# Kernel tuning notes

Measured on AMD Instinct MI355X. Metric: run time of the kernel, lower is better.

## Reference

```python
import jax, jax.numpy as jnp
import numpy as np

K_LAYERS = 10
ALPHA = 0.1
N_NODES = 100_000
N_EDGES = 1_600_000
D_FEAT = 64


def setup_inputs() -> dict:
    key = jax.random.key(0)
    k1, k2, k3 = jax.random.split(key, 3)
    features = jax.random.normal(k1, (N_NODES, D_FEAT), dtype=jnp.float32)
    src = jax.random.randint(k2, (N_EDGES,), 0, N_NODES, dtype=jnp.int64)
    dst = jax.random.randint(k3, (N_EDGES,), 0, N_NODES, dtype=jnp.int64)
    return {"features": features, "src": src, "dst": dst}


def reference(features, src, dst):
    # APPNP forward (eval mode: feature dropout and edge_drop are identity).
    n = features.shape[0]
    ones = jnp.ones((src.shape[0],), dtype=features.dtype)
    deg_out = jax.ops.segment_sum(ones, src, num_segments=n)
    deg_in = jax.ops.segment_sum(ones, dst, num_segments=n)
    norm_src = jnp.clip(deg_out, 1.0) ** -0.5  # [N]
    norm_dst = jnp.clip(deg_in, 1.0) ** -0.5   # [N]

    h0 = features
    h = features
    for _ in range(K_LAYERS):
        # D_out^{-1/2} scaling, gather to edges, scatter-sum to dst, D_in^{-1/2}
        msg = (h * norm_src[:, None])[src]               # [E, d]
        agg = jax.ops.segment_sum(msg, dst, num_segments=n)  # [N, d]
        h = (1.0 - ALPHA) * (agg * norm_dst[:, None]) + ALPHA * h0
    return h
```

## Files before the change

kernel.cpp:

```cpp
#include <hip/hip_runtime.h>
#include <hip/hip_fp16.h>
#include <stdint.h>

#define D_FEAT 64
#define K_LAYERS 10
#define SCAN_CHUNK 2048

__global__ void deg_kernel(const int* __restrict__ src, const int* __restrict__ dst,
                           int* deg_out, int* deg_in, int* __restrict__ rank, int E) {
    int i = blockIdx.x * blockDim.x + threadIdx.x;
    int base = i * 4;
    if (base + 3 < E) {
        int4 s4 = *(const int4*)(src + base);
        int4 d4 = *(const int4*)(dst + base);
        atomicAdd(&deg_out[s4.x], 1);
        atomicAdd(&deg_out[s4.y], 1);
        atomicAdd(&deg_out[s4.z], 1);
        atomicAdd(&deg_out[s4.w], 1);
        int4 r;
        r.x = atomicAdd(&deg_in[d4.x], 1);
        r.y = atomicAdd(&deg_in[d4.y], 1);
        r.z = atomicAdd(&deg_in[d4.z], 1);
        r.w = atomicAdd(&deg_in[d4.w], 1);
        *(int4*)(rank + base) = r;
    } else {
        for (int j = base; j < E; ++j) {
            atomicAdd(&deg_out[src[j]], 1);
            rank[j] = atomicAdd(&deg_in[dst[j]], 1);
        }
    }
}

__global__ void norm_kernel(const int* __restrict__ deg_out, const int* __restrict__ deg_in,
                            float* __restrict__ ns, float* __restrict__ nd,
                            float* __restrict__ cvec, int N) {
    int i = blockIdx.x * blockDim.x + threadIdx.x;
    if (i < N) {
        float a = rsqrtf(fmaxf((float)deg_out[i], 1.0f));
        float b = rsqrtf(fmaxf((float)deg_in[i], 1.0f));
        ns[i] = a;
        nd[i] = b;
        cvec[i] = 0.9f * a * b;
    }
}

__global__ void chunk_sum_kernel(const int* __restrict__ deg, int N, int* __restrict__ partials) {
    __shared__ int sdata[256];
    constexpr int PT = SCAN_CHUNK / 256;
    int base = blockIdx.x * SCAN_CHUNK;
    int t = threadIdx.x;
    int s = 0;
#pragma unroll
    for (int j = 0; j < PT; ++j) {
        int idx = base + t * PT + j;
        if (idx < N) s += deg[idx];
    }
    sdata[t] = s;
    __syncthreads();
    for (int off = 128; off > 0; off >>= 1) {
        if (t < off) sdata[t] += sdata[t + off];
        __syncthreads();
    }
    if (t == 0) partials[blockIdx.x] = sdata[0];
}

__global__ void scan_partials_kernel(int* partials, int nchunks, int* row_ptr, int N, int E) {
    if (threadIdx.x == 0 && blockIdx.x == 0) {
        int s = 0;
        for (int i = 0; i < nchunks; ++i) { int v = partials[i]; partials[i] = s; s += v; }
        row_ptr[N] = E;
    }
}

__global__ void chunk_scan_kernel(const int* __restrict__ deg, int N,
                                  const int* __restrict__ partials, int* __restrict__ row_ptr) {
    __shared__ int sdata[256];
    constexpr int PT = SCAN_CHUNK / 256;
    int base = blockIdx.x * SCAN_CHUNK;
    int t = threadIdx.x;
    int vals[PT];
    int s = 0;
#pragma unroll
    for (int j = 0; j < PT; ++j) {
        int idx = base + t * PT + j;
        int v = (idx < N) ? deg[idx] : 0;
        vals[j] = s;
        s += v;
    }
    sdata[t] = s;
    __syncthreads();
    for (int off = 1; off < 256; off <<= 1) {
        int v = (t >= off) ? sdata[t - off] : 0;
        __syncthreads();
        sdata[t] += v;
        __syncthreads();
    }
    int texcl = (t > 0) ? sdata[t - 1] : 0;
    int off0 = partials[blockIdx.x];
#pragma unroll
    for (int j = 0; j < PT; ++j) {
        int idx = base + t * PT + j;
        if (idx < N) row_ptr[idx] = off0 + texcl + vals[j];
    }
}

__global__ void fill_cvt_kernel(const int* __restrict__ src, const int* __restrict__ dst,
                                const int* __restrict__ rank, const int* __restrict__ row_ptr,
                                unsigned* __restrict__ edge_src, int E, int fillBlocks,
                                const float* __restrict__ features, const float* __restrict__ ns,
                                __half* __restrict__ g0, __half* __restrict__ f0g, int N) {
    int b = blockIdx.x;
    if (b < fillBlocks) {
        int i = b * blockDim.x + threadIdx.x;
        int base = i * 4;
        if (base + 3 < E) {
            int4 s4 = *(const int4*)(src + base);
            int4 d4 = *(const int4*)(dst + base);
            int4 r4 = *(const int4*)(rank + base);
            edge_src[row_ptr[d4.x] + r4.x] = (unsigned)s4.x;
            edge_src[row_ptr[d4.y] + r4.y] = (unsigned)s4.y;
            edge_src[row_ptr[d4.z] + r4.z] = (unsigned)s4.z;
            edge_src[row_ptr[d4.w] + r4.w] = (unsigned)s4.w;
        } else {
            for (int j = base; j < E; ++j)
                edge_src[row_ptr[dst[j]] + rank[j]] = (unsigned)src[j];
        }
    } else {
        int t = (b - fillBlocks) * blockDim.x + threadIdx.x;
        if (t < N * (D_FEAT / 8)) {
            int node = t >> 3;
            float s = ns[node];
            float4 a = *((const float4*)features + 2 * t);
            float4 c = *((const float4*)features + 2 * t + 1);
            __half2 og[4], of[4];
        og[0] = __float22half2_rn(make_float2(s * a.x, s * a.y));
        og[1] = __float22half2_rn(make_float2(s * a.z, s * a.w));
        og[2] = __float22half2_rn(make_float2(s * c.x, s * c.y));
        og[3] = __float22half2_rn(make_float2(s * c.z, s * c.w));
        float sf = 0.1f * s;
        of[0] = __float22half2_rn(make_float2(sf * a.x, sf * a.y));
        of[1] = __float22half2_rn(make_float2(sf * a.z, sf * a.w));
        of[2] = __float22half2_rn(make_float2(sf * c.x, sf * c.y));
        of[3] = __float22half2_rn(make_float2(sf * c.z, sf * c.w));
            *((float4*)g0 + t)  = *(const float4*)og;
            *((float4*)f0g + t) = *(const float4*)of;
        }
    }
}

template <bool LAST>
__global__ __launch_bounds__(256) void prop_kernel(
    const __half* __restrict__ g, const __half* __restrict__ f0g,
    const float* __restrict__ features,
    const unsigned* __restrict__ edge_src, const int* __restrict__ row_ptr,
    const float* __restrict__ cvec, const float* __restrict__ nd,
    void* __restrict__ out, int N)
{
    int gid  = blockIdx.x * blockDim.x + threadIdx.x;
    int node = gid >> 6;
    if (node >= N) return;
    int lane = threadIdx.x & 63;
    int grp  = lane >> 3;
    int fl   = lane & 7;

    int start = row_ptr[node];
    int end   = row_ptr[node + 1];

    float acc[8];
#pragma unroll
    for (int j = 0; j < 8; ++j) acc[j] = 0.f;

    int e = start + grp;
    for (; e + 8 < end; e += 16) {
        unsigned s0 = edge_src[e];
        unsigned s1 = edge_src[e + 8];
        float4 v0 = *((const float4*)(g + ((size_t)s0 << 6)) + fl);
        float4 v1 = *((const float4*)(g + ((size_t)s1 << 6)) + fl);
        const __half2* p0 = (const __half2*)&v0;
        const __half2* p1 = (const __half2*)&v1;
#pragma unroll
        for (int k = 0; k < 4; ++k) {
            float2 f0 = __half22float2(p0[k]);
            float2 f1 = __half22float2(p1[k]);
            acc[2 * k]     += f0.x + f1.x;
            acc[2 * k + 1] += f0.y + f1.y;
        }
    }
    if (e < end) {
        unsigned s0 = edge_src[e];
        float4 v0 = *((const float4*)(g + ((size_t)s0 << 6)) + fl);
        const __half2* p0 = (const __half2*)&v0;
#pragma unroll
        for (int k = 0; k < 4; ++k) {
            float2 f0 = __half22float2(p0[k]);
            acc[2 * k]     += f0.x;
            acc[2 * k + 1] += f0.y;
        }
    }

#pragma unroll
    for (int j = 0; j < 8; ++j) acc[j] += __shfl_xor(acc[j], 8, 64);
#pragma unroll
    for (int j = 0; j < 8; ++j) acc[j] += __shfl_xor(acc[j], 16, 64);
#pragma unroll
    for (int j = 0; j < 8; ++j) acc[j] += __shfl_xor(acc[j], 32, 64);

    if (grp == 0) {
        if (!LAST) {
            float cm = cvec[node];
            float4 braw = *((const float4*)(f0g + ((size_t)node << 6)) + fl);
            const __half2* bp = (const __half2*)&braw;
            __half2 o[4];
#pragma unroll
            for (int k = 0; k < 4; ++k) {
                float2 f = __half22float2(bp[k]);
                o[k] = __float22half2_rn(make_float2(fmaf(cm, acc[2 * k], f.x),
                                                     fmaf(cm, acc[2 * k + 1], f.y)));
            }
            *((float4*)((__half*)out + ((size_t)node << 6)) + fl) = *(const float4*)o;
        } else {
            float w = 0.9f * nd[node];
            const float4* fp = (const float4*)(features + ((size_t)node << 6));
            float4 b0 = fp[2 * fl];
            float4 b1 = fp[2 * fl + 1];
            float4 o0, o1;
            o0.x = fmaf(w, acc[0], 0.1f * b0.x);
            o0.y = fmaf(w, acc[1], 0.1f * b0.y);
            o0.z = fmaf(w, acc[2], 0.1f * b0.z);
            o0.w = fmaf(w, acc[3], 0.1f * b0.w);
            o1.x = fmaf(w, acc[4], 0.1f * b1.x);
            o1.y = fmaf(w, acc[5], 0.1f * b1.y);
            o1.z = fmaf(w, acc[6], 0.1f * b1.z);
            o1.w = fmaf(w, acc[7], 0.1f * b1.w);
            float4* op = (float4*)((float*)out + ((size_t)node << 6));
            op[2 * fl]     = o0;
            op[2 * fl + 1] = o1;
        }
    }
}

extern "C" void kernel_launch(void* const* d_in, const int* in_sizes, int n_in,
                              void* d_out, int out_size, void* d_ws, size_t ws_size,
                              hipStream_t stream) {
    const float* features = (const float*)d_in[0];
    const int*   src      = (const int*)d_in[1];
    const int*   dst      = (const int*)d_in[2];
    const int E = in_sizes[1];
    const int N = in_sizes[0] / D_FEAT;

    char* ws = (char*)d_ws;
    size_t off = 0;
    auto alloc = [&](size_t bytes, size_t align) -> char* {
        off = (off + align - 1) & ~(align - 1);
        char* p = ws + off;
        off += bytes;
        return p;
    };
    int*      deg_out  = (int*)alloc(4 * (size_t)N, 4);
    int*      deg_in   = (int*)alloc(4 * (size_t)N, 4);
    int*      row_ptr  = (int*)alloc(4 * ((size_t)N + 1), 4);
    float*    ns       = (float*)alloc(4 * (size_t)N, 4);
    float*    nd       = (float*)alloc(4 * (size_t)N, 4);
    float*    cvec     = (float*)alloc(4 * (size_t)N, 4);
    int nchunks = (N + SCAN_CHUNK - 1) / SCAN_CHUNK;
    int*      partials = (int*)alloc(4 * (size_t)nchunks, 4);
    int*      rank     = (int*)alloc(4 * (size_t)E, 16);
    unsigned* edge_src = (unsigned*)alloc(4 * (size_t)E, 16);
    __half*   f0g      = (__half*)alloc(2 * (size_t)N * D_FEAT, 16);
    __half*   gA       = (__half*)alloc(2 * (size_t)N * D_FEAT, 16);
    __half*   gB       = (__half*)alloc(2 * (size_t)N * D_FEAT, 16);

    hipMemsetAsync(deg_out, 0, 4 * (size_t)N * 2, stream);

    int ethreads4 = (E + 3) / 4;
    int eblocks = (ethreads4 + 255) / 256;
    deg_kernel<<<eblocks, 256, 0, stream>>>(src, dst, deg_out, deg_in, rank, E);
    norm_kernel<<<(N + 255) / 256, 256, 0, stream>>>(deg_out, deg_in, ns, nd, cvec, N);
    chunk_sum_kernel<<<nchunks, 256, 0, stream>>>(deg_in, N, partials);
    scan_partials_kernel<<<1, 64, 0, stream>>>(partials, nchunks, row_ptr, N, E);
    chunk_scan_kernel<<<nchunks, 256, 0, stream>>>(deg_in, N, partials, row_ptr);

    int cvtThreads = N * (D_FEAT / 8);
    int cvtBlocks = (cvtThreads + 255) / 256;
    fill_cvt_kernel<<<eblocks + cvtBlocks, 256, 0, stream>>>(
        src, dst, rank, row_ptr, edge_src, E, eblocks, features, ns, gA, f0g, N);

    int prop_blocks = (int)(((size_t)N * 64 + 255) / 256);
    const __half* h_in = gA;
    for (int k = 0; k < K_LAYERS - 1; ++k) {
        __half* h_out = (k & 1) ? gA : gB;
        prop_kernel<false><<<prop_blocks, 256, 0, stream>>>(
            h_in, f0g, features, edge_src, row_ptr, cvec, nd, h_out, N);
        h_in = h_out;
    }
    prop_kernel<true><<<prop_blocks, 256, 0, stream>>>(
        h_in, f0g, features, edge_src, row_ptr, cvec, nd, d_out, N);
}
```

Measured before the change: 728.8 us.

## Use LDS histogram for out-degree and map one node per 8-lane group

Out-degree counting moves from global atomics to 32 dedicated blocks that build per-block LDS histograms over node ranges, writing partial counts that norm_kernel sums. The in-degree and rank atomics run in other blocks of the same launch. The propagation kernel now gives each 8-lane group its own node instead of a whole 64-lane wave per node, which removes the cross-group shuffle reduction and the idle lanes on nodes with few edges. In exchange, it adds a 32×N partials buffer, repeated passes over the src stripes, and more load imbalance within a wave.

```diff
diff --git a/kernel.cpp b/kernel.cpp
--- a/kernel.cpp
+++ b/kernel.cpp
@@ -5,42 +5,76 @@
 #define D_FEAT 64
 #define K_LAYERS 10
 #define SCAN_CHUNK 2048
-
-__global__ void deg_kernel(const int* __restrict__ src, const int* __restrict__ dst,
-                           int* deg_out, int* deg_in, int* __restrict__ rank, int E) {
-    int i = blockIdx.x * blockDim.x + threadIdx.x;
-    int base = i * 4;
-    if (base + 3 < E) {
-        int4 s4 = *(const int4*)(src + base);
-        int4 d4 = *(const int4*)(dst + base);
-        atomicAdd(&deg_out[s4.x], 1);
-        atomicAdd(&deg_out[s4.y], 1);
-        atomicAdd(&deg_out[s4.z], 1);
-        atomicAdd(&deg_out[s4.w], 1);
-        int4 r;
-        r.x = atomicAdd(&deg_in[d4.x], 1);
-        r.y = atomicAdd(&deg_in[d4.y], 1);
-        r.z = atomicAdd(&deg_in[d4.z], 1);
-        r.w = atomicAdd(&deg_in[d4.w], 1);
-        *(int4*)(rank + base) = r;
+#define HIST_BLOCKS 32
+#define HIST_RANGE 16384
+
+__global__ void deg_hist_kernel(const int* __restrict__ src, const int* __restrict__ dst,
+                                int* deg_in, int* __restrict__ rank,
+                                unsigned* __restrict__ partials, int E, int histBlocks, int N) {
+    __shared__ unsigned lds[HIST_RANGE];
+    int b = blockIdx.x;
+    if (b >= histBlocks) {
+        int i = (b - histBlocks) * blockDim.x + threadIdx.x;
+        int base = i * 4;
+        if (base + 3 < E) {
+            int4 d4 = *(const int4*)(dst + base);
+            int4 r;
+            r.x = atomicAdd(&deg_in[d4.x], 1);
+            r.y = atomicAdd(&deg_in[d4.y], 1);
+            r.z = atomicAdd(&deg_in[d4.z], 1);
+            r.w = atomicAdd(&deg_in[d4.w], 1);
+            *(int4*)(rank + base) = r;
+        } else {
+            for (int j = base; j < E; ++j)
+                rank[j] = atomicAdd(&deg_in[dst[j]], 1);
+        }
     } else {
-        for (int j = base; j < E; ++j) {
-            atomicAdd(&deg_out[src[j]], 1);
-            rank[j] = atomicAdd(&deg_in[dst[j]], 1);
-        }
-    }
-}
-
-__global__ void norm_kernel(const int* __restrict__ deg_out, const int* __restrict__ deg_in,
+        int stripe = ((E + histBlocks - 1) / histBlocks + 3) & ~3;
+        int begin = b * stripe;
+        int endb  = min(E, begin + stripe);
+        int nr = (N + HIST_RANGE - 1) / HIST_RANGE;
+        for (int r = 0; r < nr; ++r) {
+            for (int j = threadIdx.x; j < HIST_RANGE; j += blockDim.x) lds[j] = 0;
+            __syncthreads();
+            unsigned lo = (unsigned)(r * HIST_RANGE);
+            for (int p = begin + (int)threadIdx.x * 4; p < endb; p += blockDim.x * 4) {
+                if (p + 3 < endb) {
+                    int4 s4 = *(const int4*)(src + p);
+                    unsigned k;
+                    k = (unsigned)s4.x - lo; if (k < HIST_RANGE) atomicAdd(&lds[k], 1u);
+                    k = (unsigned)s4.y - lo; if (k < HIST_RANGE) atomicAdd(&lds[k], 1u);
+                    k = (unsigned)s4.z - lo; if (k < HIST_RANGE) atomicAdd(&lds[k], 1u);
+                    k = (unsigned)s4.w - lo; if (k < HIST_RANGE) atomicAdd(&lds[k], 1u);
+                } else {
+                    for (int q = p; q < endb; ++q) {
+                        unsigned k = (unsigned)src[q] - lo;
+                        if (k < HIST_RANGE) atomicAdd(&lds[k], 1u);
+                    }
+                }
+            }
+            __syncthreads();
+            for (int j = threadIdx.x; j < HIST_RANGE; j += blockDim.x) {
+                int gi = r * HIST_RANGE + j;
+                if (gi < N) partials[(size_t)b * N + gi] = lds[j];
+            }
+            __syncthreads();
+        }
+    }
+}
+
+__global__ void norm_kernel(const unsigned* __restrict__ partials, const int* __restrict__ deg_in,
                             float* __restrict__ ns, float* __restrict__ nd,
                             float* __restrict__ cvec, int N) {
     int i = blockIdx.x * blockDim.x + threadIdx.x;
     if (i < N) {
-        float a = rsqrtf(fmaxf((float)deg_out[i], 1.0f));
-        float b = rsqrtf(fmaxf((float)deg_in[i], 1.0f));
+        unsigned s = 0;
+#pragma unroll 8
+        for (int b = 0; b < HIST_BLOCKS; ++b) s += partials[(size_t)b * N + i];
+        float a = rsqrtf(fmaxf((float)s, 1.0f));
+        float bb = rsqrtf(fmaxf((float)deg_in[i], 1.0f));
         ns[i] = a;
-        nd[i] = b;
-        cvec[i] = 0.9f * a * b;
+        nd[i] = bb;
+        cvec[i] = 0.9f * a * bb;
     }
 }
 
@@ -133,15 +167,15 @@
             float4 a = *((const float4*)features + 2 * t);
             float4 c = *((const float4*)features + 2 * t + 1);
             __half2 og[4], of[4];
-        og[0] = __float22half2_rn(make_float2(s * a.x, s * a.y));
-        og[1] = __float22half2_rn(make_float2(s * a.z, s * a.w));
-        og[2] = __float22half2_rn(make_float2(s * c.x, s * c.y));
-        og[3] = __float22half2_rn(make_float2(s * c.z, s * c.w));
-        float sf = 0.1f * s;
-        of[0] = __float22half2_rn(make_float2(sf * a.x, sf * a.y));
-        of[1] = __float22half2_rn(make_float2(sf * a.z, sf * a.w));
-        of[2] = __float22half2_rn(make_float2(sf * c.x, sf * c.y));
-        of[3] = __float22half2_rn(make_float2(sf * c.z, sf * c.w));
+            og[0] = __float22half2_rn(make_float2(s * a.x, s * a.y));
+            og[1] = __float22half2_rn(make_float2(s * a.z, s * a.w));
+            og[2] = __float22half2_rn(make_float2(s * c.x, s * c.y));
+            og[3] = __float22half2_rn(make_float2(s * c.z, s * c.w));
+            float sf = 0.1f * s;
+            of[0] = __float22half2_rn(make_float2(sf * a.x, sf * a.y));
+            of[1] = __float22half2_rn(make_float2(sf * a.z, sf * a.w));
+            of[2] = __float22half2_rn(make_float2(sf * c.x, sf * c.y));
+            of[3] = __float22half2_rn(make_float2(sf * c.z, sf * c.w));
             *((float4*)g0 + t)  = *(const float4*)og;
             *((float4*)f0g + t) = *(const float4*)of;
         }
@@ -156,24 +190,24 @@
     const float* __restrict__ cvec, const float* __restrict__ nd,
     void* __restrict__ out, int N)
 {
-    int gid  = blockIdx.x * blockDim.x + threadIdx.x;
-    int node = gid >> 6;
-    if (node >= N) return;
+    int tid  = blockIdx.x * blockDim.x + threadIdx.x;
+    int wave = tid >> 6;
     int lane = threadIdx.x & 63;
     int grp  = lane >> 3;
     int fl   = lane & 7;
-
-    int start = row_ptr[node];
-    int end   = row_ptr[node + 1];
+    int node = wave * 8 + grp;
+    if (node >= N) return;
+
+    int e   = row_ptr[node];
+    int end = row_ptr[node + 1];
 
     float acc[8];
 #pragma unroll
     for (int j = 0; j < 8; ++j) acc[j] = 0.f;
 
-    int e = start + grp;
-    for (; e + 8 < end; e += 16) {
+    for (; e + 2 <= end; e += 2) {
         unsigned s0 = edge_src[e];
-        unsigned s1 = edge_src[e + 8];
+        unsigned s1 = edge_src[e + 1];
         float4 v0 = *((const float4*)(g + ((size_t)s0 << 6)) + fl);
         float4 v1 = *((const float4*)(g + ((size_t)s1 << 6)) + fl);
         const __half2* p0 = (const __half2*)&v0;
@@ -198,44 +232,35 @@
         }
     }
 
-#pragma unroll
-    for (int j = 0; j < 8; ++j) acc[j] += __shfl_xor(acc[j], 8, 64);
-#pragma unroll
-    for (int j = 0; j < 8; ++j) acc[j] += __shfl_xor(acc[j], 16, 64);
-#pragma unroll
-    for (int j = 0; j < 8; ++j) acc[j] += __shfl_xor(acc[j], 32, 64);
-
-    if (grp == 0) {
-        if (!LAST) {
-            float cm = cvec[node];
-            float4 braw = *((const float4*)(f0g + ((size_t)node << 6)) + fl);
-            const __half2* bp = (const __half2*)&braw;
-            __half2 o[4];
-#pragma unroll
-            for (int k = 0; k < 4; ++k) {
-                float2 f = __half22float2(bp[k]);
-                o[k] = __float22half2_rn(make_float2(fmaf(cm, acc[2 * k], f.x),
-                                                     fmaf(cm, acc[2 * k + 1], f.y)));
-            }
-            *((float4*)((__half*)out + ((size_t)node << 6)) + fl) = *(const float4*)o;
-        } else {
-            float w = 0.9f * nd[node];
-            const float4* fp = (const float4*)(features + ((size_t)node << 6));
-            float4 b0 = fp[2 * fl];
-            float4 b1 = fp[2 * fl + 1];
-            float4 o0, o1;
-            o0.x = fmaf(w, acc[0], 0.1f * b0.x);
-            o0.y = fmaf(w, acc[1], 0.1f * b0.y);
-            o0.z = fmaf(w, acc[2], 0.1f * b0.z);
-            o0.w = fmaf(w, acc[3], 0.1f * b0.w);
-            o1.x = fmaf(w, acc[4], 0.1f * b1.x);
-            o1.y = fmaf(w, acc[5], 0.1f * b1.y);
-            o1.z = fmaf(w, acc[6], 0.1f * b1.z);
-            o1.w = fmaf(w, acc[7], 0.1f * b1.w);
-            float4* op = (float4*)((float*)out + ((size_t)node << 6));
-            op[2 * fl]     = o0;
-            op[2 * fl + 1] = o1;
-        }
+    if (!LAST) {
+        float cm = cvec[node];
+        float4 braw = *((const float4*)(f0g + ((size_t)node << 6)) + fl);
+        const __half2* bp = (const __half2*)&braw;
+        __half2 o[4];
+#pragma unroll
+        for (int k = 0; k < 4; ++k) {
+            float2 f = __half22float2(bp[k]);
+            o[k] = __float22half2_rn(make_float2(fmaf(cm, acc[2 * k], f.x),
+                                                 fmaf(cm, acc[2 * k + 1], f.y)));
+        }
+        *((float4*)((__half*)out + ((size_t)node << 6)) + fl) = *(const float4*)o;
+    } else {
+        float w = 0.9f * nd[node];
+        const float4* fp = (const float4*)(features + ((size_t)node << 6));
+        float4 b0 = fp[2 * fl];
+        float4 b1 = fp[2 * fl + 1];
+        float4 o0, o1;
+        o0.x = fmaf(w, acc[0], 0.1f * b0.x);
+        o0.y = fmaf(w, acc[1], 0.1f * b0.y);
+        o0.z = fmaf(w, acc[2], 0.1f * b0.z);
+        o0.w = fmaf(w, acc[3], 0.1f * b0.w);
+        o1.x = fmaf(w, acc[4], 0.1f * b1.x);
+        o1.y = fmaf(w, acc[5], 0.1f * b1.y);
+        o1.z = fmaf(w, acc[6], 0.1f * b1.z);
+        o1.w = fmaf(w, acc[7], 0.1f * b1.w);
+        float4* op = (float4*)((float*)out + ((size_t)node << 6));
+        op[2 * fl]     = o0;
+        op[2 * fl + 1] = o1;
     }
 }
 
@@ -256,36 +281,38 @@
         off += bytes;
         return p;
     };
-    int*      deg_out  = (int*)alloc(4 * (size_t)N, 4);
-    int*      deg_in   = (int*)alloc(4 * (size_t)N, 4);
-    int*      row_ptr  = (int*)alloc(4 * ((size_t)N + 1), 4);
-    float*    ns       = (float*)alloc(4 * (size_t)N, 4);
-    float*    nd       = (float*)alloc(4 * (size_t)N, 4);
-    float*    cvec     = (float*)alloc(4 * (size_t)N, 4);
+    int*      deg_in    = (int*)alloc(4 * (size_t)N, 4);
+    int*      row_ptr   = (int*)alloc(4 * ((size_t)N + 1), 4);
+    float*    ns        = (float*)alloc(4 * (size_t)N, 4);
+    float*    nd        = (float*)alloc(4 * (size_t)N, 4);
+    float*    cvec      = (float*)alloc(4 * (size_t)N, 4);
     int nchunks = (N + SCAN_CHUNK - 1) / SCAN_CHUNK;
-    int*      partials = (int*)alloc(4 * (size_t)nchunks, 4);
-    int*      rank     = (int*)alloc(4 * (size_t)E, 16);
-    unsigned* edge_src = (unsigned*)alloc(4 * (size_t)E, 16);
-    __half*   f0g      = (__half*)alloc(2 * (size_t)N * D_FEAT, 16);
-    __half*   gA       = (__half*)alloc(2 * (size_t)N * D_FEAT, 16);
-    __half*   gB       = (__half*)alloc(2 * (size_t)N * D_FEAT, 16);
-
-    hipMemsetAsync(deg_out, 0, 4 * (size_t)N * 2, stream);
+    int*      spartials = (int*)alloc(4 * (size_t)nchunks, 4);
+    unsigned* hpartials = (unsigned*)alloc(4 * (size_t)HIST_BLOCKS * N, 16);
+    int*      rank      = (int*)alloc(4 * (size_t)E, 16);
+    unsigned* edge_src  = (unsigned*)alloc(4 * (size_t)E, 16);
+    __half*   f0g       = (__half*)alloc(2 * (size_t)N * D_FEAT, 16);
+    __half*   gA        = (__half*)alloc(2 * (size_t)N * D_FEAT, 16);
+    __half*   gB        = (__half*)alloc(2 * (size_t)N * D_FEAT, 16);
+
+    hipMemsetAsync(deg_in, 0, 4 * (size_t)N, stream);
 
     int ethreads4 = (E + 3) / 4;
     int eblocks = (ethreads4 + 255) / 256;
-    deg_kernel<<<eblocks, 256, 0, stream>>>(src, dst, deg_out, deg_in, rank, E);
-    norm_kernel<<<(N + 255) / 256, 256, 0, stream>>>(deg_out, deg_in, ns, nd, cvec, N);
-    chunk_sum_kernel<<<nchunks, 256, 0, stream>>>(deg_in, N, partials);
-    scan_partials_kernel<<<1, 64, 0, stream>>>(partials, nchunks, row_ptr, N, E);
-    chunk_scan_kernel<<<nchunks, 256, 0, stream>>>(deg_in, N, partials, row_ptr);
+    deg_hist_kernel<<<HIST_BLOCKS + eblocks, 256, 0, stream>>>(
+        src, dst, deg_in, rank, hpartials, E, HIST_BLOCKS, N);
+    norm_kernel<<<(N + 255) / 256, 256, 0, stream>>>(hpartials, deg_in, ns, nd, cvec, N);
+    chunk_sum_kernel<<<nchunks, 256, 0, stream>>>(deg_in, N, spartials);
+    scan_partials_kernel<<<1, 64, 0, stream>>>(spartials, nchunks, row_ptr, N, E);
+    chunk_scan_kernel<<<nchunks, 256, 0, stream>>>(deg_in, N, spartials, row_ptr);
 
     int cvtThreads = N * (D_FEAT / 8);
     int cvtBlocks = (cvtThreads + 255) / 256;
     fill_cvt_kernel<<<eblocks + cvtBlocks, 256, 0, stream>>>(
         src, dst, rank, row_ptr, edge_src, E, eblocks, features, ns, gA, f0g, N);
 
-    int prop_blocks = (int)(((size_t)N * 64 + 255) / 256);
+    int waves = (N + 7) / 8;
+    int prop_blocks = (waves * 64 + 255) / 256;
     const __half* h_in = gA;
     for (int k = 0; k < K_LAYERS - 1; ++k) {
         __half* h_out = (k & 1) ? gA : gB;
```

Measured after the change: 777.4 us. +6.7%, slower.

## Map one node per 8-lane group instead of one node per wavefront

Applied to the files above, without the earlier changes.

The propagation kernel now assigns each 8-lane group its own destination node, so a wavefront handles 8 nodes. This removes the cross-group shuffle reduction and the idle lanes during the epilogue. The edge loop is templated on an unroll factor, with layers alternating between 2 and 4 loads in flight. The cost is load imbalance between nodes of different degree inside one wave, and fewer independent gathers per node than the old 16-edge stride.

```diff
diff --git a/kernel.cpp b/kernel.cpp
--- a/kernel.cpp
+++ b/kernel.cpp
@@ -133,22 +133,22 @@
             float4 a = *((const float4*)features + 2 * t);
             float4 c = *((const float4*)features + 2 * t + 1);
             __half2 og[4], of[4];
-        og[0] = __float22half2_rn(make_float2(s * a.x, s * a.y));
-        og[1] = __float22half2_rn(make_float2(s * a.z, s * a.w));
-        og[2] = __float22half2_rn(make_float2(s * c.x, s * c.y));
-        og[3] = __float22half2_rn(make_float2(s * c.z, s * c.w));
-        float sf = 0.1f * s;
-        of[0] = __float22half2_rn(make_float2(sf * a.x, sf * a.y));
-        of[1] = __float22half2_rn(make_float2(sf * a.z, sf * a.w));
-        of[2] = __float22half2_rn(make_float2(sf * c.x, sf * c.y));
-        of[3] = __float22half2_rn(make_float2(sf * c.z, sf * c.w));
+            og[0] = __float22half2_rn(make_float2(s * a.x, s * a.y));
+            og[1] = __float22half2_rn(make_float2(s * a.z, s * a.w));
+            og[2] = __float22half2_rn(make_float2(s * c.x, s * c.y));
+            og[3] = __float22half2_rn(make_float2(s * c.z, s * c.w));
+            float sf = 0.1f * s;
+            of[0] = __float22half2_rn(make_float2(sf * a.x, sf * a.y));
+            of[1] = __float22half2_rn(make_float2(sf * a.z, sf * a.w));
+            of[2] = __float22half2_rn(make_float2(sf * c.x, sf * c.y));
+            of[3] = __float22half2_rn(make_float2(sf * c.z, sf * c.w));
             *((float4*)g0 + t)  = *(const float4*)og;
             *((float4*)f0g + t) = *(const float4*)of;
         }
     }
 }
 
-template <bool LAST>
+template <bool LAST, int ILP>
 __global__ __launch_bounds__(256) void prop_kernel(
     const __half* __restrict__ g, const __half* __restrict__ f0g,
     const float* __restrict__ features,
@@ -156,37 +156,41 @@
     const float* __restrict__ cvec, const float* __restrict__ nd,
     void* __restrict__ out, int N)
 {
-    int gid  = blockIdx.x * blockDim.x + threadIdx.x;
-    int node = gid >> 6;
-    if (node >= N) return;
+    int tid  = blockIdx.x * blockDim.x + threadIdx.x;
+    int wave = tid >> 6;
     int lane = threadIdx.x & 63;
     int grp  = lane >> 3;
     int fl   = lane & 7;
-
-    int start = row_ptr[node];
-    int end   = row_ptr[node + 1];
+    int node = wave * 8 + grp;
+    if (node >= N) return;
+
+    int e   = row_ptr[node];
+    int end = row_ptr[node + 1];
 
     float acc[8];
 #pragma unroll
     for (int j = 0; j < 8; ++j) acc[j] = 0.f;
 
-    int e = start + grp;
-    for (; e + 8 < end; e += 16) {
-        unsigned s0 = edge_src[e];
-        unsigned s1 = edge_src[e + 8];
-        float4 v0 = *((const float4*)(g + ((size_t)s0 << 6)) + fl);
-        float4 v1 = *((const float4*)(g + ((size_t)s1 << 6)) + fl);
-        const __half2* p0 = (const __half2*)&v0;
-        const __half2* p1 = (const __half2*)&v1;
-#pragma unroll
-        for (int k = 0; k < 4; ++k) {
-            float2 f0 = __half22float2(p0[k]);
-            float2 f1 = __half22float2(p1[k]);
-            acc[2 * k]     += f0.x + f1.x;
-            acc[2 * k + 1] += f0.y + f1.y;
-        }
-    }
-    if (e < end) {
+    for (; e + ILP <= end; e += ILP) {
+        unsigned s[ILP];
+        float4 v[ILP];
+#pragma unroll
+        for (int u = 0; u < ILP; ++u) s[u] = edge_src[e + u];
+#pragma unroll
+        for (int u = 0; u < ILP; ++u)
+            v[u] = *((const float4*)(g + ((size_t)s[u] << 6)) + fl);
+#pragma unroll
+        for (int u = 0; u < ILP; ++u) {
+            const __half2* p = (const __half2*)&v[u];
+#pragma unroll
+            for (int k = 0; k < 4; ++k) {
+                float2 f = __half22float2(p[k]);
+                acc[2 * k]     += f.x;
+                acc[2 * k + 1] += f.y;
+            }
+        }
+    }
+    for (; e < end; ++e) {
         unsigned s0 = edge_src[e];
         float4 v0 = *((const float4*)(g + ((size_t)s0 << 6)) + fl);
         const __half2* p0 = (const __half2*)&v0;
@@ -198,44 +202,35 @@
         }
     }
 
-#pragma unroll
-    for (int j = 0; j < 8; ++j) acc[j] += __shfl_xor(acc[j], 8, 64);
-#pragma unroll
-    for (int j = 0; j < 8; ++j) acc[j] += __shfl_xor(acc[j], 16, 64);
-#pragma unroll
-    for (int j = 0; j < 8; ++j) acc[j] += __shfl_xor(acc[j], 32, 64);
-
-    if (grp == 0) {
-        if (!LAST) {
-            float cm = cvec[node];
-            float4 braw = *((const float4*)(f0g + ((size_t)node << 6)) + fl);
-            const __half2* bp = (const __half2*)&braw;
-            __half2 o[4];
-#pragma unroll
-            for (int k = 0; k < 4; ++k) {
-                float2 f = __half22float2(bp[k]);
-                o[k] = __float22half2_rn(make_float2(fmaf(cm, acc[2 * k], f.x),
-                                                     fmaf(cm, acc[2 * k + 1], f.y)));
-            }
-            *((float4*)((__half*)out + ((size_t)node << 6)) + fl) = *(const float4*)o;
-        } else {
-            float w = 0.9f * nd[node];
-            const float4* fp = (const float4*)(features + ((size_t)node << 6));
-            float4 b0 = fp[2 * fl];
-            float4 b1 = fp[2 * fl + 1];
-            float4 o0, o1;
-            o0.x = fmaf(w, acc[0], 0.1f * b0.x);
-            o0.y = fmaf(w, acc[1], 0.1f * b0.y);
-            o0.z = fmaf(w, acc[2], 0.1f * b0.z);
-            o0.w = fmaf(w, acc[3], 0.1f * b0.w);
-            o1.x = fmaf(w, acc[4], 0.1f * b1.x);
-            o1.y = fmaf(w, acc[5], 0.1f * b1.y);
-            o1.z = fmaf(w, acc[6], 0.1f * b1.z);
-            o1.w = fmaf(w, acc[7], 0.1f * b1.w);
-            float4* op = (float4*)((float*)out + ((size_t)node << 6));
-            op[2 * fl]     = o0;
-            op[2 * fl + 1] = o1;
-        }
+    if (!LAST) {
+        float cm = cvec[node];
+        float4 braw = *((const float4*)(f0g + ((size_t)node << 6)) + fl);
+        const __half2* bp = (const __half2*)&braw;
+        __half2 o[4];
+#pragma unroll
+        for (int k = 0; k < 4; ++k) {
+            float2 f = __half22float2(bp[k]);
+            o[k] = __float22half2_rn(make_float2(fmaf(cm, acc[2 * k], f.x),
+                                                 fmaf(cm, acc[2 * k + 1], f.y)));
+        }
+        *((float4*)((__half*)out + ((size_t)node << 6)) + fl) = *(const float4*)o;
+    } else {
+        float w = 0.9f * nd[node];
+        const float4* fp = (const float4*)(features + ((size_t)node << 6));
+        float4 b0 = fp[2 * fl];
+        float4 b1 = fp[2 * fl + 1];
+        float4 o0, o1;
+        o0.x = fmaf(w, acc[0], 0.1f * b0.x);
+        o0.y = fmaf(w, acc[1], 0.1f * b0.y);
+        o0.z = fmaf(w, acc[2], 0.1f * b0.z);
+        o0.w = fmaf(w, acc[3], 0.1f * b0.w);
+        o1.x = fmaf(w, acc[4], 0.1f * b1.x);
+        o1.y = fmaf(w, acc[5], 0.1f * b1.y);
+        o1.z = fmaf(w, acc[6], 0.1f * b1.z);
+        o1.w = fmaf(w, acc[7], 0.1f * b1.w);
+        float4* op = (float4*)((float*)out + ((size_t)node << 6));
+        op[2 * fl]     = o0;
+        op[2 * fl + 1] = o1;
     }
 }
 
@@ -263,7 +258,7 @@
     float*    nd       = (float*)alloc(4 * (size_t)N, 4);
     float*    cvec     = (float*)alloc(4 * (size_t)N, 4);
     int nchunks = (N + SCAN_CHUNK - 1) / SCAN_CHUNK;
-    int*      partials = (int*)alloc(4 * (size_t)nchunks, 4);
+    int*      spartials = (int*)alloc(4 * (size_t)nchunks, 4);
     int*      rank     = (int*)alloc(4 * (size_t)E, 16);
     unsigned* edge_src = (unsigned*)alloc(4 * (size_t)E, 16);
     __half*   f0g      = (__half*)alloc(2 * (size_t)N * D_FEAT, 16);
@@ -276,23 +271,28 @@
     int eblocks = (ethreads4 + 255) / 256;
     deg_kernel<<<eblocks, 256, 0, stream>>>(src, dst, deg_out, deg_in, rank, E);
     norm_kernel<<<(N + 255) / 256, 256, 0, stream>>>(deg_out, deg_in, ns, nd, cvec, N);
-    chunk_sum_kernel<<<nchunks, 256, 0, stream>>>(deg_in, N, partials);
-    scan_partials_kernel<<<1, 64, 0, stream>>>(partials, nchunks, row_ptr, N, E);
-    chunk_scan_kernel<<<nchunks, 256, 0, stream>>>(deg_in, N, partials, row_ptr);
+    chunk_sum_kernel<<<nchunks, 256, 0, stream>>>(deg_in, N, spartials);
+    scan_partials_kernel<<<1, 64, 0, stream>>>(spartials, nchunks, row_ptr, N, E);
+    chunk_scan_kernel<<<nchunks, 256, 0, stream>>>(deg_in, N, spartials, row_ptr);
 
     int cvtThreads = N * (D_FEAT / 8);
     int cvtBlocks = (cvtThreads + 255) / 256;
     fill_cvt_kernel<<<eblocks + cvtBlocks, 256, 0, stream>>>(
         src, dst, rank, row_ptr, edge_src, E, eblocks, features, ns, gA, f0g, N);
 
-    int prop_blocks = (int)(((size_t)N * 64 + 255) / 256);
+    int waves = (N + 7) / 8;
+    int prop_blocks = (waves * 64 + 255) / 256;
     const __half* h_in = gA;
     for (int k = 0; k < K_LAYERS - 1; ++k) {
         __half* h_out = (k & 1) ? gA : gB;
-        prop_kernel<false><<<prop_blocks, 256, 0, stream>>>(
-            h_in, f0g, features, edge_src, row_ptr, cvec, nd, h_out, N);
+        if (k & 1)
+            prop_kernel<false, 4><<<prop_blocks, 256, 0, stream>>>(
+                h_in, f0g, features, edge_src, row_ptr, cvec, nd, h_out, N);
+        else
+            prop_kernel<false, 2><<<prop_blocks, 256, 0, stream>>>(
+                h_in, f0g, features, edge_src, row_ptr, cvec, nd, h_out, N);
         h_in = h_out;
     }
-    prop_kernel<true><<<prop_blocks, 256, 0, stream>>>(
+    prop_kernel<true, 2><<<prop_blocks, 256, 0, stream>>>(
         h_in, f0g, features, edge_src, row_ptr, cvec, nd, d_out, N);
 }
```

After: 720.9 us. No clear change (-1.1%).
